# Kernel tuning notes

Measured on AMD Instinct MI355X. Metric: run time of the kernel, lower is better.

## Reference

```python
import jax, jax.numpy as jnp
import numpy as np

D_MODEL = 1024
NUM_HEADS = 16
HEAD_DIM = D_MODEL // NUM_HEADS
B, L = 2, 2048


def setup_inputs() -> dict:
    key = jax.random.key(0)
    ks = jax.random.split(key, 9)
    s = 0.02
    return {
        "query": jax.random.normal(ks[0], (B, L, D_MODEL), dtype=jnp.float32),
        "key": jax.random.normal(ks[1], (B, L, D_MODEL), dtype=jnp.float32),
        "value": jax.random.normal(ks[2], (B, L, D_MODEL), dtype=jnp.float32),
        "mask": jax.random.randint(ks[3], (B, L), 0, 2, dtype=jnp.int32),
        "Wq": jax.random.normal(ks[4], (D_MODEL, D_MODEL), dtype=jnp.float32) * s,
        "Wk": jax.random.normal(ks[5], (D_MODEL, D_MODEL), dtype=jnp.float32) * s,
        "Wv": jax.random.normal(ks[6], (D_MODEL, D_MODEL), dtype=jnp.float32) * s,
        "Wo": jax.random.normal(ks[7], (D_MODEL, D_MODEL), dtype=jnp.float32) * s,
        "bo": jnp.zeros((D_MODEL,), dtype=jnp.float32),
    }


def _split_heads(x):
    # (B, L, d_model) -> (B, H, L, head_dim)
    b, l, _ = x.shape
    return x.reshape(b, l, NUM_HEADS, HEAD_DIM).transpose(0, 2, 1, 3)


def reference(query, key, value, mask, Wq, Wk, Wv, Wo, bo):
    # nn.Linear(bias=False): x @ W.T
    q = _split_heads(query @ Wq.T)   # (B, H, L, hd)
    k = _split_heads(key @ Wk.T)
    v = _split_heads(value @ Wv.T)

    scores = jnp.einsum("bhqd,bhkd->bhqk", q, k) / jnp.sqrt(jnp.float32(HEAD_DIM))
    # padding mask over keys: (B, L) -> (B, 1, 1, L); 0 = pad -> -inf
    keep = (mask[:, None, None, :] != 0)
    scores = jnp.where(keep, scores, -jnp.inf)

    attn = jax.nn.softmax(scores, axis=-1)
    # original zeroes NaN rows (fully-masked query rows)
    attn = jnp.where(jnp.isnan(attn), jnp.zeros_like(attn), attn)
    # dropout is identity in eval/reference mode

    ctx = jnp.einsum("bhqk,bhkd->bhqd", attn, v)           # (B, H, L, hd)
    ctx = ctx.transpose(0, 2, 1, 3).reshape(B, L, D_MODEL)  # combine heads
    return ctx @ Wo.T + bo
```

## Files before the change

kernel.cpp:

```cpp
#include <hip/hip_runtime.h>

typedef unsigned short u16;
typedef __bf16 bf16x8 __attribute__((ext_vector_type(8)));
typedef __bf16 bf16x4 __attribute__((ext_vector_type(4)));
typedef float floatx4 __attribute__((ext_vector_type(4)));
typedef u16 u16x4 __attribute__((ext_vector_type(4)));

#define MEG ((size_t)(1u << 20))

__device__ __forceinline__ u16 f2bf(float f) {
  unsigned int u = __float_as_uint(f);
  u += 0x7fffu + ((u >> 16) & 1u);
  return (u16)(u >> 16);
}

__device__ __forceinline__ void load_lds16(const u16* g, u16* l) {
  __builtin_amdgcn_global_load_lds((const __attribute__((address_space(1))) unsigned int*)g,
                                   (__attribute__((address_space(3))) unsigned int*)l,
                                   16, 0, 0);
}

__global__ __launch_bounds__(256) void cvt7(
    const float* __restrict__ s0, const float* __restrict__ s1,
    const float* __restrict__ s2, const float* __restrict__ s3,
    const float* __restrict__ s4, const float* __restrict__ s5,
    const float* __restrict__ s6, u16* __restrict__ dst)
{
  size_t e = ((size_t)blockIdx.x * 256 + threadIdx.x) * 4;
  unsigned m = (unsigned)(e >> 20);
  const float* s; size_t off;
  if (m < 4)       { s = s0; off = e; }
  else if (m < 8)  { s = s1; off = e - 4 * MEG; }
  else if (m < 12) { s = s2; off = e - 8 * MEG; }
  else if (m < 13) { s = s3; off = e - 12 * MEG; }
  else if (m < 14) { s = s4; off = e - 13 * MEG; }
  else if (m < 15) { s = s5; off = e - 14 * MEG; }
  else             { s = s6; off = e - 15 * MEG; }
  float4 f = *reinterpret_cast<const float4*>(s + off);
  u16x4 o;
  o.x = f2bf(f.x); o.y = f2bf(f.y); o.z = f2bf(f.z); o.w = f2bf(f.w);
  *reinterpret_cast<u16x4*>(dst + e) = o;
}

template<bool OUT_BF16, bool ADD_BIAS>
__global__ __launch_bounds__(256) void gemm_bt(
    const u16* __restrict__ Abase, const u16* __restrict__ Bbase,
    const float* __restrict__ bias, void* __restrict__ Cbase,
    int M, int N, int K, long zA, long zB, long zC)
{
  __shared__ __align__(16) u16 As[128 * 64];
  __shared__ __align__(16) u16 Bs[128 * 64];
  const int tid = threadIdx.x;
  const int w = tid >> 6, ln = tid & 63;
  const int lm = ln & 15, lq = ln >> 4;
  const int wm = w >> 1, wn = w & 1;
  const long m0 = (long)blockIdx.y * 128, n0 = (long)blockIdx.x * 128;
  const u16* A = Abase + (size_t)blockIdx.z * (size_t)zA;
  const u16* B = Bbase + (size_t)blockIdx.z * (size_t)zB;

  const int r0 = tid >> 3;
  const int kc = (tid & 7) ^ (r0 & 7);
  const u16* gA = A + (m0 + r0) * (long)K + kc * 8;
  const u16* gB = B + (n0 + r0) * (long)K + kc * 8;
  const long rstep = 32L * K;

  const int sl0 = (lq ^ (lm & 7)) * 8;
  const int sl1 = ((4 + lq) ^ (lm & 7)) * 8;
  const u16* ab0 = &As[(wm * 64 + lm) * 64 + sl0];
  const u16* ab1 = &As[(wm * 64 + lm) * 64 + sl1];
  const u16* bb0 = &Bs[(wn * 64 + lm) * 64 + sl0];
  const u16* bb1 = &Bs[(wn * 64 + lm) * 64 + sl1];

  const floatx4 z4 = {0.f, 0.f, 0.f, 0.f};
  floatx4 acc[4][4];
#pragma unroll
  for (int i = 0; i < 4; ++i)
#pragma unroll
    for (int j = 0; j < 4; ++j) acc[i][j] = z4;

  for (int k0 = 0; k0 < K; k0 += 64) {
#pragma unroll
    for (int t = 0; t < 4; ++t) {
      load_lds16(gA + t * rstep, &As[(t * 256 + w * 64) * 8]);
      load_lds16(gB + t * rstep, &Bs[(t * 256 + w * 64) * 8]);
    }
    gA += 64; gB += 64;
    __syncthreads();
    bf16x8 af[4][2], bfr[4][2];
#pragma unroll
    for (int i = 0; i < 4; ++i) {
      af[i][0] = *reinterpret_cast<const bf16x8*>(ab0 + i * 1024);
      af[i][1] = *reinterpret_cast<const bf16x8*>(ab1 + i * 1024);
    }
#pragma unroll
    for (int j = 0; j < 4; ++j) {
      bfr[j][0] = *reinterpret_cast<const bf16x8*>(bb0 + j * 1024);
      bfr[j][1] = *reinterpret_cast<const bf16x8*>(bb1 + j * 1024);
    }
#pragma unroll
    for (int i = 0; i < 4; ++i)
#pragma unroll
      for (int j = 0; j < 4; ++j) {
        acc[i][j] = __builtin_amdgcn_mfma_f32_16x16x32_bf16(af[i][0], bfr[j][0], acc[i][j], 0, 0, 0);
        acc[i][j] = __builtin_amdgcn_mfma_f32_16x16x32_bf16(af[i][1], bfr[j][1], acc[i][j], 0, 0, 0);
      }
    __syncthreads();
  }

#pragma unroll
  for (int i = 0; i < 4; ++i) {
    long row = m0 + wm * 64 + i * 16 + lq * 4;
#pragma unroll
    for (int j = 0; j < 4; ++j) {
      long col = n0 + wn * 64 + j * 16 + lm;
#pragma unroll
      for (int r = 0; r < 4; ++r) {
        float v = acc[i][j][r];
        if (ADD_BIAS) v += bias[col];
        size_t idx = (size_t)(row + r) * (size_t)N + (size_t)col;
        if (OUT_BF16) (((u16*)Cbase) + (size_t)blockIdx.z * (size_t)zC)[idx] = f2bf(v);
        else ((float*)Cbase)[idx] = v;
      }
    }
  }
}

__global__ __launch_bounds__(256) void transpose_v(const u16* __restrict__ Vp, u16* __restrict__ Vt)
{
  __shared__ u16 T[64 * 80];
  const int tid = threadIdx.x;
  const int bh = blockIdx.y, b = bh >> 4, h = bh & 15;
  const int l0 = blockIdx.x * 64;
#pragma unroll
  for (int t = 0; t < 2; ++t) {
    int ci = t * 256 + tid;
    int l = ci >> 3, c = ci & 7;
    *reinterpret_cast<uint4*>(&T[l * 80 + c * 8]) =
      *reinterpret_cast<const uint4*>(&Vp[((size_t)(b * 2048 + l0 + l)) * 1024 + h * 64 + c * 8]);
  }
  __syncthreads();
#pragma unroll
  for (int t = 0; t < 2; ++t) {
    int ci = t * 256 + tid;
    int d = ci >> 3, lg = ci & 7;
    u16 tmp[8];
#pragma unroll
    for (int s = 0; s < 8; ++s) tmp[s] = T[(lg * 8 + s) * 80 + d];
    *reinterpret_cast<uint4*>(&Vt[(size_t)bh * 131072 + (size_t)d * 2048 + l0 + lg * 8]) =
      *reinterpret_cast<uint4*>(tmp);
  }
}

__global__ __launch_bounds__(256, 4) void attn_kernel(
    const u16* __restrict__ Qp, const u16* __restrict__ Kp,
    const u16* __restrict__ Vt, const int* __restrict__ mask,
    u16* __restrict__ ctx)
{
  __shared__ __align__(16) u16 Ks[64 * 64];
  __shared__ __align__(16) u16 Vts[64 * 64];
  __shared__ __align__(16) u16 Ps[4 * 16 * 64];
  __shared__ __align__(16) float mball[2048];

  const int tid = threadIdx.x;
  const int w = tid >> 6, ln = tid & 63;
  const int lm = ln & 15, lq = ln >> 4;
  const int bh = blockIdx.y, b = bh >> 4, h = bh & 15;
  const int q0 = blockIdx.x * 64;

  const u16* Qh = Qp + (size_t)b * 2048 * 1024 + h * 64;
  const u16* Kh = Kp + (size_t)b * 2048 * 1024 + h * 64;
  const u16* Vth = Vt + (size_t)bh * 64 * 2048;

  const int* mrow = mask + b * 2048;
#pragma unroll
  for (int t = 0; t < 8; ++t) {
    int i = t * 256 + tid;
    mball[i] = (mrow[i] != 0) ? 0.f : -1e30f;
  }

  const int qrow = q0 + w * 16 + lm;
  bf16x8 qf0 = *reinterpret_cast<const bf16x8*>(Qh + (size_t)qrow * 1024 + lq * 8);
  bf16x8 qf1 = *reinterpret_cast<const bf16x8*>(Qh + (size_t)qrow * 1024 + 32 + lq * 8);

  const int sl0 = (lq ^ (lm & 7)) * 8;
  const int sl1 = ((4 + lq) ^ (lm & 7)) * 8;
  const u16* kb0 = &Ks[lm * 64 + sl0];
  const u16* kb1 = &Ks[lm * 64 + sl1];
  const u16* vb0 = &Vts[lm * 64 + sl0];
  const u16* vb1 = &Vts[lm * 64 + sl1];
  u16* Pw = &Ps[w * 1024];
  u16* pwr[4];
#pragma unroll
  for (int n = 0; n < 4; ++n) pwr[n] = &Pw[lm * 64 + (((4 * n + lq) ^ lm) * 4)];
  const u16* prd[4];
#pragma unroll
  for (int t = 0; t < 4; ++t)
    prd[t] = &Pw[lm * 64 + (((8 * (t >> 1) + 2 * lq + (t & 1)) ^ lm) * 4)];
  const float* mbi = mball + lq * 4;

  const int r0 = tid >> 3;
  const int kc = (tid & 7) ^ (r0 & 7);
  const u16* gK0 = Kh + (size_t)r0 * 1024 + kc * 8;
  const u16* gK1 = gK0 + 32 * 1024;
  const u16* gV0 = Vth + (size_t)r0 * 2048 + kc * 8;
  const u16* gV1 = gV0 + 32 * 2048;

  const floatx4 z4 = {0.f, 0.f, 0.f, 0.f};
  floatx4 O[4];
#pragma unroll
  for (int j = 0; j < 4; ++j) O[j] = z4;
  float psum = 0.f;
  const float SCL = 0.18033688011112042f;

  for (int it = 0; it < 32; ++it) {
    load_lds16(gK0, &Ks[(w * 64) * 8]);
    load_lds16(gK1, &Ks[(256 + w * 64) * 8]);
    load_lds16(gV0, &Vts[(w * 64) * 8]);
    load_lds16(gV1, &Vts[(256 + w * 64) * 8]);
    gK0 += 64 * 1024; gK1 += 64 * 1024; gV0 += 64; gV1 += 64;
    __syncthreads();

    bf16x8 kf[4][2];
#pragma unroll
    for (int n = 0; n < 4; ++n) {
      kf[n][0] = *reinterpret_cast<const bf16x8*>(kb0 + n * 1024);
      kf[n][1] = *reinterpret_cast<const bf16x8*>(kb1 + n * 1024);
    }
    floatx4 S[4];
#pragma unroll
    for (int n = 0; n < 4; ++n) {
      S[n] = __builtin_amdgcn_mfma_f32_16x16x32_bf16(kf[n][0], qf0, z4, 0, 0, 0);
      S[n] = __builtin_amdgcn_mfma_f32_16x16x32_bf16(kf[n][1], qf1, S[n], 0, 0, 0);
    }

#pragma unroll
    for (int n = 0; n < 4; ++n) {
      float4 m4 = *reinterpret_cast<const float4*>(mbi + n * 16);
      float p0 = __builtin_amdgcn_exp2f(fmaf(S[n][0], SCL, m4.x));
      float p1 = __builtin_amdgcn_exp2f(fmaf(S[n][1], SCL, m4.y));
      float p2 = __builtin_amdgcn_exp2f(fmaf(S[n][2], SCL, m4.z));
      float p3 = __builtin_amdgcn_exp2f(fmaf(S[n][3], SCL, m4.w));
      psum += (p0 + p1) + (p2 + p3);
      unsigned u0 = __float_as_uint(p0) + 0x8000u;
      unsigned u1 = __float_as_uint(p1) + 0x8000u;
      unsigned u2 = __float_as_uint(p2) + 0x8000u;
      unsigned u3 = __float_as_uint(p3) + 0x8000u;
      uint2 pk;
      pk.x = __builtin_amdgcn_perm(u1, u0, 0x07060302u);
      pk.y = __builtin_amdgcn_perm(u3, u2, 0x07060302u);
      *reinterpret_cast<uint2*>(pwr[n]) = pk;
    }

#pragma unroll
    for (int h2 = 0; h2 < 2; ++h2) {
      bf16x4 pa = *reinterpret_cast<const bf16x4*>(prd[2 * h2]);
      bf16x4 pb = *reinterpret_cast<const bf16x4*>(prd[2 * h2 + 1]);
      bf16x8 pf = __builtin_shufflevector(pa, pb, 0, 1, 2, 3, 4, 5, 6, 7);
      const u16* vb = (h2 == 0) ? vb0 : vb1;
#pragma unroll
      for (int j = 0; j < 4; ++j) {
        bf16x8 vf = *reinterpret_cast<const bf16x8*>(vb + j * 1024);
        O[j] = __builtin_amdgcn_mfma_f32_16x16x32_bf16(pf, vf, O[j], 0, 0, 0);
      }
    }
    mbi += 64;
    __syncthreads();
  }

  float s = psum;
  s += __shfl_xor(s, 16, 64);
  s += __shfl_xor(s, 32, 64);
#pragma unroll
  for (int r = 0; r < 4; ++r) {
    int srcl = (ln & 48) | (lq * 4 + r);
    float inv = 1.0f / __shfl(s, srcl, 64);
    int row = q0 + w * 16 + lq * 4 + r;
    size_t base = ((size_t)b * 2048 + row) * 1024 + h * 64 + lm;
#pragma unroll
    for (int j = 0; j < 4; ++j)
      ctx[base + j * 16] = f2bf(O[j][r] * inv);
  }
}

extern "C" void kernel_launch(void* const* d_in, const int* in_sizes, int n_in,
                              void* d_out, int out_size, void* d_ws, size_t ws_size,
                              hipStream_t stream) {
  const float* q  = (const float*)d_in[0];
  const float* k  = (const float*)d_in[1];
  const float* v  = (const float*)d_in[2];
  const int*   mk = (const int*)  d_in[3];
  const float* wq = (const float*)d_in[4];
  const float* wk = (const float*)d_in[5];
  const float* wv = (const float*)d_in[6];
  const float* wo = (const float*)d_in[7];
  const float* bo = (const float*)d_in[8];

  u16* ws16 = (u16*)d_ws;
  u16* Xq  = ws16;
  u16* Wq  = ws16 + 12 * MEG;
  u16* Wo  = ws16 + 15 * MEG;
  u16* Qp  = ws16 + 16 * MEG;
  u16* Kp  = ws16 + 20 * MEG;
  u16* Vp  = ws16 + 24 * MEG;
  u16* Vt  = ws16;
  u16* ctx = ws16 + 4 * MEG;

  cvt7<<<dim3(16384), dim3(256), 0, stream>>>(q, k, v, wq, wk, wv, wo, ws16);

  gemm_bt<true, false><<<dim3(8, 32, 3), dim3(256), 0, stream>>>(
      Xq, Wq, nullptr, (void*)Qp, 4096, 1024, 1024,
      (long)(4 * MEG), (long)MEG, (long)(4 * MEG));

  transpose_v<<<dim3(32, 32), dim3(256), 0, stream>>>(Vp, Vt);

  attn_kernel<<<dim3(32, 32), dim3(256), 0, stream>>>(Qp, Kp, Vt, mk, ctx);

  gemm_bt<false, true><<<dim3(8, 32, 1), dim3(256), 0, stream>>>(
      ctx, Wo, bo, d_out, 4096, 1024, 1024, 0, 0, 0);
}
```

Baseline: 239.2 us.

## Process two query tiles per attention warp and shrink output GEMM M-tile

The attention kernel now gives each warp 32 query rows (two 16-row sub-tiles), so every block covers 128 queries. Each K/V tile loaded into LDS is reused for twice the work, and the grid and per-block K/V traffic are halved. The launch bound drops to 2 blocks per SM to leave room for the larger register footprint. The GEMM is templated on the M-tile size, and the output projection uses 64-row tiles to double its block count on a grid that was otherwise small.

```diff
diff --git a/kernel.cpp b/kernel.cpp
--- a/kernel.cpp
+++ b/kernel.cpp
@@ -42,19 +42,19 @@
   *reinterpret_cast<u16x4*>(dst + e) = o;
 }
 
-template<bool OUT_BF16, bool ADD_BIAS>
+template<int IT, bool OUT_BF16, bool ADD_BIAS>
 __global__ __launch_bounds__(256) void gemm_bt(
     const u16* __restrict__ Abase, const u16* __restrict__ Bbase,
     const float* __restrict__ bias, void* __restrict__ Cbase,
     int M, int N, int K, long zA, long zB, long zC)
 {
-  __shared__ __align__(16) u16 As[128 * 64];
+  __shared__ __align__(16) u16 As[IT * 32 * 64];
   __shared__ __align__(16) u16 Bs[128 * 64];
   const int tid = threadIdx.x;
   const int w = tid >> 6, ln = tid & 63;
   const int lm = ln & 15, lq = ln >> 4;
   const int wm = w >> 1, wn = w & 1;
-  const long m0 = (long)blockIdx.y * 128, n0 = (long)blockIdx.x * 128;
+  const long m0 = (long)blockIdx.y * (IT * 32), n0 = (long)blockIdx.x * 128;
   const u16* A = Abase + (size_t)blockIdx.z * (size_t)zA;
   const u16* B = Bbase + (size_t)blockIdx.z * (size_t)zB;
 
@@ -66,29 +66,30 @@
 
   const int sl0 = (lq ^ (lm & 7)) * 8;
   const int sl1 = ((4 + lq) ^ (lm & 7)) * 8;
-  const u16* ab0 = &As[(wm * 64 + lm) * 64 + sl0];
-  const u16* ab1 = &As[(wm * 64 + lm) * 64 + sl1];
+  const u16* ab0 = &As[(wm * (IT * 16) + lm) * 64 + sl0];
+  const u16* ab1 = &As[(wm * (IT * 16) + lm) * 64 + sl1];
   const u16* bb0 = &Bs[(wn * 64 + lm) * 64 + sl0];
   const u16* bb1 = &Bs[(wn * 64 + lm) * 64 + sl1];
 
   const floatx4 z4 = {0.f, 0.f, 0.f, 0.f};
-  floatx4 acc[4][4];
-#pragma unroll
-  for (int i = 0; i < 4; ++i)
+  floatx4 acc[IT][4];
+#pragma unroll
+  for (int i = 0; i < IT; ++i)
 #pragma unroll
     for (int j = 0; j < 4; ++j) acc[i][j] = z4;
 
   for (int k0 = 0; k0 < K; k0 += 64) {
 #pragma unroll
-    for (int t = 0; t < 4; ++t) {
+    for (int t = 0; t < IT; ++t)
       load_lds16(gA + t * rstep, &As[(t * 256 + w * 64) * 8]);
+#pragma unroll
+    for (int t = 0; t < 4; ++t)
       load_lds16(gB + t * rstep, &Bs[(t * 256 + w * 64) * 8]);
-    }
     gA += 64; gB += 64;
     __syncthreads();
-    bf16x8 af[4][2], bfr[4][2];
-#pragma unroll
-    for (int i = 0; i < 4; ++i) {
+    bf16x8 af[IT][2], bfr[4][2];
+#pragma unroll
+    for (int i = 0; i < IT; ++i) {
       af[i][0] = *reinterpret_cast<const bf16x8*>(ab0 + i * 1024);
       af[i][1] = *reinterpret_cast<const bf16x8*>(ab1 + i * 1024);
     }
@@ -98,7 +99,7 @@
       bfr[j][1] = *reinterpret_cast<const bf16x8*>(bb1 + j * 1024);
     }
 #pragma unroll
-    for (int i = 0; i < 4; ++i)
+    for (int i = 0; i < IT; ++i)
 #pragma unroll
       for (int j = 0; j < 4; ++j) {
         acc[i][j] = __builtin_amdgcn_mfma_f32_16x16x32_bf16(af[i][0], bfr[j][0], acc[i][j], 0, 0, 0);
@@ -108,8 +109,8 @@
   }
 
 #pragma unroll
-  for (int i = 0; i < 4; ++i) {
-    long row = m0 + wm * 64 + i * 16 + lq * 4;
+  for (int i = 0; i < IT; ++i) {
+    long row = m0 + wm * (IT * 16) + i * 16 + lq * 4;
 #pragma unroll
     for (int j = 0; j < 4; ++j) {
       long col = n0 + wn * 64 + j * 16 + lm;
@@ -151,36 +152,40 @@
   }
 }
 
-__global__ __launch_bounds__(256, 4) void attn_kernel(
+__global__ __launch_bounds__(256, 2) void attn_kernel(
     const u16* __restrict__ Qp, const u16* __restrict__ Kp,
     const u16* __restrict__ Vt, const int* __restrict__ mask,
     u16* __restrict__ ctx)
 {
   __shared__ __align__(16) u16 Ks[64 * 64];
   __shared__ __align__(16) u16 Vts[64 * 64];
-  __shared__ __align__(16) u16 Ps[4 * 16 * 64];
+  __shared__ __align__(16) u16 Ps[4 * 32 * 64];
   __shared__ __align__(16) float mball[2048];
 
   const int tid = threadIdx.x;
   const int w = tid >> 6, ln = tid & 63;
   const int lm = ln & 15, lq = ln >> 4;
   const int bh = blockIdx.y, b = bh >> 4, h = bh & 15;
-  const int q0 = blockIdx.x * 64;
+  const int q0 = blockIdx.x * 128;
 
   const u16* Qh = Qp + (size_t)b * 2048 * 1024 + h * 64;
   const u16* Kh = Kp + (size_t)b * 2048 * 1024 + h * 64;
   const u16* Vth = Vt + (size_t)bh * 64 * 2048;
 
-  const int* mrow = mask + b * 2048;
+  const int* mrowp = mask + b * 2048;
 #pragma unroll
   for (int t = 0; t < 8; ++t) {
     int i = t * 256 + tid;
-    mball[i] = (mrow[i] != 0) ? 0.f : -1e30f;
-  }
-
-  const int qrow = q0 + w * 16 + lm;
-  bf16x8 qf0 = *reinterpret_cast<const bf16x8*>(Qh + (size_t)qrow * 1024 + lq * 8);
-  bf16x8 qf1 = *reinterpret_cast<const bf16x8*>(Qh + (size_t)qrow * 1024 + 32 + lq * 8);
+    mball[i] = (mrowp[i] != 0) ? 0.f : -1e30f;
+  }
+
+  bf16x8 qf[2][2];
+#pragma unroll
+  for (int m = 0; m < 2; ++m) {
+    int qrow = q0 + w * 32 + m * 16 + lm;
+    qf[m][0] = *reinterpret_cast<const bf16x8*>(Qh + (size_t)qrow * 1024 + lq * 8);
+    qf[m][1] = *reinterpret_cast<const bf16x8*>(Qh + (size_t)qrow * 1024 + 32 + lq * 8);
+  }
 
   const int sl0 = (lq ^ (lm & 7)) * 8;
   const int sl1 = ((4 + lq) ^ (lm & 7)) * 8;
@@ -188,7 +193,7 @@
   const u16* kb1 = &Ks[lm * 64 + sl1];
   const u16* vb0 = &Vts[lm * 64 + sl0];
   const u16* vb1 = &Vts[lm * 64 + sl1];
-  u16* Pw = &Ps[w * 1024];
+  u16* Pw = &Ps[w * 2048];
   u16* pwr[4];
 #pragma unroll
   for (int n = 0; n < 4; ++n) pwr[n] = &Pw[lm * 64 + (((4 * n + lq) ^ lm) * 4)];
@@ -206,10 +211,12 @@
   const u16* gV1 = gV0 + 32 * 2048;
 
   const floatx4 z4 = {0.f, 0.f, 0.f, 0.f};
-  floatx4 O[4];
-#pragma unroll
-  for (int j = 0; j < 4; ++j) O[j] = z4;
-  float psum = 0.f;
+  floatx4 O[2][4];
+#pragma unroll
+  for (int m = 0; m < 2; ++m)
+#pragma unroll
+    for (int j = 0; j < 4; ++j) O[m][j] = z4;
+  float psum[2] = {0.f, 0.f};
   const float SCL = 0.18033688011112042f;
 
   for (int it = 0; it < 32; ++it) {
@@ -220,65 +227,74 @@
     gK0 += 64 * 1024; gK1 += 64 * 1024; gV0 += 64; gV1 += 64;
     __syncthreads();
 
-    bf16x8 kf[4][2];
+    bf16x8 kf[4][2], vf[4][2];
 #pragma unroll
     for (int n = 0; n < 4; ++n) {
       kf[n][0] = *reinterpret_cast<const bf16x8*>(kb0 + n * 1024);
       kf[n][1] = *reinterpret_cast<const bf16x8*>(kb1 + n * 1024);
     }
-    floatx4 S[4];
-#pragma unroll
-    for (int n = 0; n < 4; ++n) {
-      S[n] = __builtin_amdgcn_mfma_f32_16x16x32_bf16(kf[n][0], qf0, z4, 0, 0, 0);
-      S[n] = __builtin_amdgcn_mfma_f32_16x16x32_bf16(kf[n][1], qf1, S[n], 0, 0, 0);
-    }
-
-#pragma unroll
-    for (int n = 0; n < 4; ++n) {
-      float4 m4 = *reinterpret_cast<const float4*>(mbi + n * 16);
-      float p0 = __builtin_amdgcn_exp2f(fmaf(S[n][0], SCL, m4.x));
-      float p1 = __builtin_amdgcn_exp2f(fmaf(S[n][1], SCL, m4.y));
-      float p2 = __builtin_amdgcn_exp2f(fmaf(S[n][2], SCL, m4.z));
-      float p3 = __builtin_amdgcn_exp2f(fmaf(S[n][3], SCL, m4.w));
-      psum += (p0 + p1) + (p2 + p3);
-      unsigned u0 = __float_as_uint(p0) + 0x8000u;
-      unsigned u1 = __float_as_uint(p1) + 0x8000u;
-      unsigned u2 = __float_as_uint(p2) + 0x8000u;
-      unsigned u3 = __float_as_uint(p3) + 0x8000u;
-      uint2 pk;
-      pk.x = __builtin_amdgcn_perm(u1, u0, 0x07060302u);
-      pk.y = __builtin_amdgcn_perm(u3, u2, 0x07060302u);
-      *reinterpret_cast<uint2*>(pwr[n]) = pk;
-    }
-
-#pragma unroll
-    for (int h2 = 0; h2 < 2; ++h2) {
-      bf16x4 pa = *reinterpret_cast<const bf16x4*>(prd[2 * h2]);
-      bf16x4 pb = *reinterpret_cast<const bf16x4*>(prd[2 * h2 + 1]);
-      bf16x8 pf = __builtin_shufflevector(pa, pb, 0, 1, 2, 3, 4, 5, 6, 7);
-      const u16* vb = (h2 == 0) ? vb0 : vb1;
-#pragma unroll
-      for (int j = 0; j < 4; ++j) {
-        bf16x8 vf = *reinterpret_cast<const bf16x8*>(vb + j * 1024);
-        O[j] = __builtin_amdgcn_mfma_f32_16x16x32_bf16(pf, vf, O[j], 0, 0, 0);
+#pragma unroll
+    for (int j = 0; j < 4; ++j) {
+      vf[j][0] = *reinterpret_cast<const bf16x8*>(vb0 + j * 1024);
+      vf[j][1] = *reinterpret_cast<const bf16x8*>(vb1 + j * 1024);
+    }
+
+#pragma unroll
+    for (int m = 0; m < 2; ++m) {
+      floatx4 S[4];
+#pragma unroll
+      for (int n = 0; n < 4; ++n) {
+        S[n] = __builtin_amdgcn_mfma_f32_16x16x32_bf16(kf[n][0], qf[m][0], z4, 0, 0, 0);
+        S[n] = __builtin_amdgcn_mfma_f32_16x16x32_bf16(kf[n][1], qf[m][1], S[n], 0, 0, 0);
+      }
+
+#pragma unroll
+      for (int n = 0; n < 4; ++n) {
+        float4 m4 = *reinterpret_cast<const float4*>(mbi + n * 16);
+        float p0 = __builtin_amdgcn_exp2f(fmaf(S[n][0], SCL, m4.x));
+        float p1 = __builtin_amdgcn_exp2f(fmaf(S[n][1], SCL, m4.y));
+        float p2 = __builtin_amdgcn_exp2f(fmaf(S[n][2], SCL, m4.z));
+        float p3 = __builtin_amdgcn_exp2f(fmaf(S[n][3], SCL, m4.w));
+        psum[m] += (p0 + p1) + (p2 + p3);
+        unsigned u0 = __float_as_uint(p0) + 0x8000u;
+        unsigned u1 = __float_as_uint(p1) + 0x8000u;
+        unsigned u2 = __float_as_uint(p2) + 0x8000u;
+        unsigned u3 = __float_as_uint(p3) + 0x8000u;
+        uint2 pk;
+        pk.x = __builtin_amdgcn_perm(u1, u0, 0x07060302u);
+        pk.y = __builtin_amdgcn_perm(u3, u2, 0x07060302u);
+        *reinterpret_cast<uint2*>(pwr[n] + m * 1024) = pk;
+      }
+
+#pragma unroll
+      for (int h2 = 0; h2 < 2; ++h2) {
+        bf16x4 pa = *reinterpret_cast<const bf16x4*>(prd[2 * h2] + m * 1024);
+        bf16x4 pb = *reinterpret_cast<const bf16x4*>(prd[2 * h2 + 1] + m * 1024);
+        bf16x8 pf = __builtin_shufflevector(pa, pb, 0, 1, 2, 3, 4, 5, 6, 7);
+#pragma unroll
+        for (int j = 0; j < 4; ++j)
+          O[m][j] = __builtin_amdgcn_mfma_f32_16x16x32_bf16(pf, vf[j][h2], O[m][j], 0, 0, 0);
       }
     }
     mbi += 64;
     __syncthreads();
   }
 
-  float s = psum;
-  s += __shfl_xor(s, 16, 64);
-  s += __shfl_xor(s, 32, 64);
-#pragma unroll
-  for (int r = 0; r < 4; ++r) {
-    int srcl = (ln & 48) | (lq * 4 + r);
-    float inv = 1.0f / __shfl(s, srcl, 64);
-    int row = q0 + w * 16 + lq * 4 + r;
-    size_t base = ((size_t)b * 2048 + row) * 1024 + h * 64 + lm;
-#pragma unroll
-    for (int j = 0; j < 4; ++j)
-      ctx[base + j * 16] = f2bf(O[j][r] * inv);
+#pragma unroll
+  for (int m = 0; m < 2; ++m) {
+    float s = psum[m];
+    s += __shfl_xor(s, 16, 64);
+    s += __shfl_xor(s, 32, 64);
+#pragma unroll
+    for (int r = 0; r < 4; ++r) {
+      int srcl = (ln & 48) | (lq * 4 + r);
+      float inv = 1.0f / __shfl(s, srcl, 64);
+      int row = q0 + w * 32 + m * 16 + lq * 4 + r;
+      size_t base = ((size_t)b * 2048 + row) * 1024 + h * 64 + lm;
+#pragma unroll
+      for (int j = 0; j < 4; ++j)
+        ctx[base + j * 16] = f2bf(O[m][j][r] * inv);
+    }
   }
 }
 
@@ -307,14 +323,14 @@
 
   cvt7<<<dim3(16384), dim3(256), 0, stream>>>(q, k, v, wq, wk, wv, wo, ws16);
 
-  gemm_bt<true, false><<<dim3(8, 32, 3), dim3(256), 0, stream>>>(
+  gemm_bt<4, true, false><<<dim3(8, 32, 3), dim3(256), 0, stream>>>(
       Xq, Wq, nullptr, (void*)Qp, 4096, 1024, 1024,
       (long)(4 * MEG), (long)MEG, (long)(4 * MEG));
 
   transpose_v<<<dim3(32, 32), dim3(256), 0, stream>>>(Vp, Vt);
 
-  attn_kernel<<<dim3(32, 32), dim3(256), 0, stream>>>(Qp, Kp, Vt, mk, ctx);
-
-  gemm_bt<false, true><<<dim3(8, 32, 1), dim3(256), 0, stream>>>(
+  attn_kernel<<<dim3(16, 32), dim3(256), 0, stream>>>(Qp, Kp, Vt, mk, ctx);
+
+  gemm_bt<2, false, true><<<dim3(8, 64, 1), dim3(256), 0, stream>>>(
       ctx, Wo, bo, d_out, 4096, 1024, 1024, 0, 0, 0);
 }
```

Result: faster. 227.2 us (-5.0%).
